# Kernel optimization log

Hardware: AMD Instinct MI355X
Metric: run time of the kernel (lower is better)

## Reference

```python
import jax, jax.numpy as jnp
import numpy as np

DIM = 7
HID = 128
BATCH = 131072
CHOL = DIM * (DIM + 1) // 2  # 28
_TRIL_R, _TRIL_C = np.tril_indices(DIM)
_DIAG = np.arange(DIM)


def _mlp(x, W1, b1, W2, b2, W3, b3):
    h = jnp.tanh(x @ W1 + b1)
    h = jnp.tanh(h @ W2 + b2)
    return h @ W3 + b3


def _build_cholesky(raw):
    # raw: [..., CHOL] -> lower-triangular L [..., DIM, DIM], softplus diagonal for positivity
    L = jnp.zeros(raw.shape[:-1] + (DIM, DIM), raw.dtype)
    L = L.at[..., _TRIL_R, _TRIL_C].set(raw)
    L = L.at[..., _DIAG, _DIAG].set(jax.nn.softplus(L[..., _DIAG, _DIAG]))
    return L


def _spd(raw):
    L = _build_cholesky(raw)
    return L @ jnp.swapaxes(L, -1, -2)  # L L^T, SPD


def setup_inputs() -> dict:
    key = jax.random.key(0)
    ks = jax.random.split(key, 20)
    s = 0.1
    f = jnp.float32
    return {
        "q": jax.random.normal(ks[0], (BATCH, DIM), f),
        "dq": jax.random.normal(ks[1], (BATCH, DIM), f),
        "ddq": jax.random.normal(ks[2], (BATCH, DIM), f),
        "mW1": jax.random.normal(ks[3], (DIM, HID), f) * s,
        "mb1": jax.random.normal(ks[4], (HID,), f) * s,
        "mW2": jax.random.normal(ks[5], (HID, HID), f) * s,
        "mb2": jax.random.normal(ks[6], (HID,), f) * s,
        "mW3": jax.random.normal(ks[7], (HID, CHOL), f) * s,
        "mb3": jax.random.normal(ks[8], (CHOL,), f) * s,
        "dW1": jax.random.normal(ks[9], (2 * DIM, HID), f) * s,
        "db1": jax.random.normal(ks[10], (HID,), f) * s,
        "dW2": jax.random.normal(ks[11], (HID, HID), f) * s,
        "db2": jax.random.normal(ks[12], (HID,), f) * s,
        "dW3": jax.random.normal(ks[13], (HID, CHOL), f) * s,
        "db3": jax.random.normal(ks[14], (CHOL,), f) * s,
        "pW1": jax.random.normal(ks[15], (DIM, HID), f) * s,
        "pb1": jax.random.normal(ks[16], (HID,), f) * s,
        "pw2": jax.random.normal(ks[17], (HID,), f) * s,
    }


def reference(q, dq, ddq, mW1, mb1, mW2, mb2, mW3, mb3,
              dW1, db1, dW2, db2, dW3, db3, pW1, pb1, pw2):
    def M_single(qi):  # qi: [DIM] -> [DIM, DIM]
        return _spd(_mlp(qi, mW1, mb1, mW2, mb2, mW3, mb3))

    # Mass matrix M(q): [B, DIM, DIM]
    Mb = _spd(_mlp(q, mW1, mb1, mW2, mb2, mW3, mb3))

    # Full batched Jacobian dM[i,k]/dq[j] -> J[b,i,k,j], replaces DIM^3 autograd.grad loop
    J = jax.vmap(jax.jacfwd(M_single))(q)  # [B, DIM, DIM, DIM]

    # Coriolis: C[b,i,j] = 0.5 * sum_k (dM_ik/dq_j + dM_ij/dq_k - dM_jk/dq_i) * dq_k
    C = 0.5 * (jnp.einsum('bikj,bk->bij', J, dq)
               + jnp.einsum('bijk,bk->bij', J, dq)
               - jnp.einsum('bjki,bk->bij', J, dq))

    # Damping D(q, dq): [B, DIM, DIM]
    Db = _spd(_mlp(jnp.concatenate([q, dq], axis=1), dW1, db1, dW2, db2, dW3, db3))

    # Convex potential (1-hidden-layer ICNN) and its gradient
    def V_single(qi):
        h = jax.nn.softplus(qi @ pW1 + pb1)
        return h @ jax.nn.softplus(pw2)

    gradV = jax.vmap(jax.grad(V_single))(q)  # [B, DIM]

    tau = (jnp.einsum('bij,bj->bi', Mb, ddq)
           + jnp.einsum('bij,bj->bi', C + Db, dq)
           + gradV)
    return tau
```

## Files before the change

### kernel.cpp

```cpp
#include <hip/hip_runtime.h>

#define DIM 7
#define HID 128
#define CHOL 28

#define GRID_A 256
#define ITER_A 16
#define GRID_B 256
#define ITER_B 4

#define PHASE_FENCE() __builtin_amdgcn_sched_barrier(0x7F)

typedef float    f32x4  __attribute__((ext_vector_type(4)));
typedef short    bf16x8 __attribute__((ext_vector_type(8)));
typedef unsigned uint4v __attribute__((ext_vector_type(4)));
typedef unsigned uint2v __attribute__((ext_vector_type(2)));

__device__ __forceinline__ float tanh_f(float x){ float e=__expf(2.f*x); return 1.f - 2.f/(e+1.f); }
__device__ __forceinline__ float sig_f(float x){ return 1.f/(1.f+__expf(-x)); }
__device__ __forceinline__ float sp_f(float x){ return fmaxf(x,0.f) + __logf(1.f+__expf(-fabsf(x))); }

__device__ __forceinline__ unsigned short f2b(float v){
  unsigned u = __float_as_uint(v);
  u += 0x7FFFu + ((u>>16)&1u);
  return (unsigned short)(u>>16);
}
__device__ __forceinline__ unsigned pk2(float a, float b){
  unsigned ua = __float_as_uint(a), ub = __float_as_uint(b);
  ua += 0x7FFFu + ((ua>>16)&1u);
  ub += 0x7FFFu + ((ub>>16)&1u);
  return (ua>>16) | (ub & 0xFFFF0000u);
}
__device__ __forceinline__ float b2f(unsigned short v){
  return __uint_as_float(((unsigned)v)<<16);
}
__device__ __forceinline__ bf16x8 as_bf(uint4v u){ union { uint4v a; bf16x8 f; } x; x.a=u; return x.f; }

__global__ void setup_frags(const float* __restrict__ mW2, const float* __restrict__ mW3,
                            const float* __restrict__ dW2, const float* __restrict__ dW3,
                            unsigned* __restrict__ ws){
  int idx = blockIdx.x*256 + threadIdx.x;
  if (idx < 8192) {
    int i2 = idx&3, f = idx>>2, l = f&63, st = f>>6;
    int s = st>>3, t = st&7;
    int k = 32*s + 8*(l>>4) + 2*i2, col = 16*t + (l&15);
    ws[idx] = pk2(mW2[k*HID+col], mW2[(k+1)*HID+col]);
  } else if (idx < 10240) {
    int j = idx-8192; int i2=j&3, f=j>>2, l=f&63, st=f>>6;
    int s = st>>1, t = st&1;
    int k = 32*s + 8*(l>>4) + 2*i2, col = 16*t + (l&15);
    float v0 = (col<CHOL) ? mW3[k*CHOL+col] : 0.f;
    float v1 = (col<CHOL) ? mW3[(k+1)*CHOL+col] : 0.f;
    ws[idx] = pk2(v0,v1);
  } else if (idx < 18432) {
    int j = idx-10240; int i2=j&3, f=j>>2, l=f&63, st=f>>6;
    int s = st>>3, t = st&7;
    int k = 32*s + 8*(l>>4) + 2*i2, col = 16*t + (l&15);
    ws[idx] = pk2(dW2[k*HID+col], dW2[(k+1)*HID+col]);
  } else if (idx < 20480) {
    int j = idx-18432; int i2=j&3, f=j>>2, l=f&63, st=f>>6;
    int s = st>>1, t = st&1;
    int k = 32*s + 8*(l>>4) + 2*i2, col = 16*t + (l&15);
    float v0 = (col<CHOL) ? dW3[k*CHOL+col] : 0.f;
    float v1 = (col<CHOL) ? dW3[(k+1)*CHOL+col] : 0.f;
    ws[idx] = pk2(v0,v1);
  }
}

__global__ __launch_bounds__(512, 2) void kernA(
    const float* __restrict__ q, const float* __restrict__ dq, const float* __restrict__ ddq,
    const float* __restrict__ mW1, const float* __restrict__ mb1,
    const float* __restrict__ mb2, const float* __restrict__ mb3,
    const float* __restrict__ pW1, const float* __restrict__ pb1, const float* __restrict__ pw2,
    const unsigned* __restrict__ ws, float* __restrict__ out)
{
  __shared__ __align__(16) unsigned short Abuf[8][2][16][HID];
  __shared__ __align__(16) uint4v W2lds[2048];
  __shared__ __align__(16) uint4v W3lds[512];
  __shared__ __align__(4)  unsigned short sbf[8][4][HID];
  __shared__ __align__(16) unsigned short rawb[8][4][CHOL][8];
  __shared__ float pW1s[DIM][HID+8];
  __shared__ float b2s[HID];
  __shared__ float b3s[CHOL];
  __shared__ float Lbs[8][4][CHOL], dLss[8][4][CHOL], dfs[8][4][CHOL];
  __shared__ float gvp2[8][4][14];
  __shared__ float wbs[8][4][DIM], ubs[8][4][DIM], vss[8][4][DIM];

  const int tid  = threadIdx.x;
  const int wid  = tid>>6;
  const int lane = tid&63;
  const int g4 = lane>>4, c = lane&15;
  const int R = lane&15, r7 = lane&7;

  if (tid < HID) b2s[tid] = mb2[tid];
  if (tid >= HID && tid < HID+CHOL) b3s[tid-HID] = mb3[tid-HID];
  for (int idx = tid; idx < DIM*HID; idx += 512) pW1s[idx>>7][idx&127] = pW1[idx];
  for (int idx = tid; idx < 2048; idx += 512) W2lds[idx] = ((const uint4v*)ws)[idx];
  for (int idx = tid; idx < 512;  idx += 512) W3lds[idx] = ((const uint4v*)(ws + 8192))[idx];

  const int u0 = 2*lane, u1 = 2*lane+1;
  float w1a[DIM], w1b[DIM], pw1a[DIM], pw1b[DIM];
#pragma unroll
  for (int j=0;j<DIM;++j){
    w1a[j]=mW1[j*HID+u0];  w1b[j]=mW1[j*HID+u1];
    pw1a[j]=pW1[j*HID+u0]; pw1b[j]=pW1[j*HID+u1];
  }
  const float b1a=mb1[u0], b1b=mb1[u1];
  const float pba=pb1[u0], pbb=pb1[u1];
  const float spa=sp_f(pw2[u0]), spb=sp_f(pw2[u1]);

  __syncthreads();

  const int kb = lane>>2;
  const int ko2 = (2*lane)&7;

  for (int it=0; it<ITER_A; ++it){
    const int ebase = (it*GRID_A + (int)blockIdx.x)*32 + wid*4;

#pragma unroll
    for (int e=0;e<4;++e){
      const float* qp = q + (long)(ebase+e)*DIM;
      float qv[DIM];
#pragma unroll
      for (int j=0;j<DIM;++j) qv[j]=qp[j];
      const int mt = e>>1, R0 = 8*(e&1);
      float z1a=b1a, z1b=b1b, zpa=pba, zpb=pbb;
#pragma unroll
      for (int j=0;j<DIM;++j){
        z1a=fmaf(qv[j],w1a[j],z1a);  z1b=fmaf(qv[j],w1b[j],z1b);
        zpa=fmaf(qv[j],pw1a[j],zpa); zpb=fmaf(qv[j],pw1b[j],zpb);
      }
      const float h1a=tanh_f(z1a), g1a=1.f-h1a*h1a;
      const float h1b=tanh_f(z1b), g1b=1.f-h1b*h1b;
      *(unsigned*)&Abuf[wid][mt][R0][8*kb + ko2] = pk2(h1a, h1b);
#pragma unroll
      for (int j=0;j<DIM;++j)
        *(unsigned*)&Abuf[wid][mt][R0+1+j][8*(kb^(1+j)) + ko2] = pk2(g1a*w1a[j], g1b*w1b[j]);
      *(unsigned*)&sbf[wid][e][u0] = pk2(sig_f(zpa)*spa, sig_f(zpb)*spb);
    }
    PHASE_FENCE();

    bf16x8 Af0[4], Af1[4];
#pragma unroll
    for (int s=0;s<4;++s){
      const int blk = 8*((4*s+g4)^r7);
      Af0[s] = *(const bf16x8*)&Abuf[wid][0][R][blk];
      Af1[s] = *(const bf16x8*)&Abuf[wid][1][R][blk];
    }
    PHASE_FENCE();

#pragma unroll
    for (int t=0;t<8;++t){
      f32x4 a0 = f32x4{0.f,0.f,0.f,0.f};
      f32x4 a1 = f32x4{0.f,0.f,0.f,0.f};
#pragma unroll
      for (int s=0;s<4;++s){
        bf16x8 B = as_bf(W2lds[(s*8+t)*64 + lane]);
        a0 = __builtin_amdgcn_mfma_f32_16x16x32_bf16(Af0[s],B,a0,0,0,0);
        a1 = __builtin_amdgcn_mfma_f32_16x16x32_bf16(Af1[s],B,a1,0,0,0);
      }
      const int col = 16*t+c;
      const int cb = col>>3, co = col&7;
      {
        const float z2  = a0[0] + b2s[col];
        const float h2o = tanh_f(z2);
        const float h2x = __shfl_xor(h2o, 16);
        const float h2  = (g4&1) ? h2x : h2o;
        const float g2  = 1.f - h2*h2;
#pragma unroll
        for (int reg=0;reg<4;++reg){
          const int Rr = 4*g4+reg;
          const int key = Rr&7;
          float v = g2*a0[reg];
          if (key==0) v = h2;
          Abuf[wid][0][Rr][8*(cb^key) + co] = f2b(v);
        }
      }
      {
        const float z2  = a1[0] + b2s[col];
        const float h2o = tanh_f(z2);
        const float h2x = __shfl_xor(h2o, 16);
        const float h2  = (g4&1) ? h2x : h2o;
        const float g2  = 1.f - h2*h2;
#pragma unroll
        for (int reg=0;reg<4;++reg){
          const int Rr = 4*g4+reg;
          const int key = Rr&7;
          float v = g2*a1[reg];
          if (key==0) v = h2;
          Abuf[wid][1][Rr][8*(cb^key) + co] = f2b(v);
        }
      }
    }
    PHASE_FENCE();

    f32x4 acc3[2][2];
#pragma unroll
    for (int a=0;a<2;++a){ acc3[a][0]=f32x4{0.f,0.f,0.f,0.f}; acc3[a][1]=f32x4{0.f,0.f,0.f,0.f}; }
#pragma unroll
    for (int s=0;s<4;++s){
      const int blk = 8*((4*s+g4)^r7);
      bf16x8 A0 = *(const bf16x8*)&Abuf[wid][0][R][blk];
      bf16x8 A1 = *(const bf16x8*)&Abuf[wid][1][R][blk];
#pragma unroll
      for (int nt=0;nt<2;++nt){
        bf16x8 B = as_bf(W3lds[(s*2+nt)*64 + lane]);
        acc3[0][nt] = __builtin_amdgcn_mfma_f32_16x16x32_bf16(A0,B,acc3[0][nt],0,0,0);
        acc3[1][nt] = __builtin_amdgcn_mfma_f32_16x16x32_bf16(A1,B,acc3[1][nt],0,0,0);
      }
    }

    if (c < 14){
      const int iv = (c<7)? c : c-7;
      const int nb = (c<7)? 0 : 64;
      float gp = 0.f;
#pragma unroll 8
      for (int nn=0; nn<32; ++nn){
        const unsigned sp2 = *(const unsigned*)&sbf[wid][g4][nb+2*nn];
        const float2 pw = *(const float2*)&pW1s[iv][nb+2*nn];
        gp = fmaf(pw.x, __uint_as_float(sp2<<16), gp);
        gp = fmaf(pw.y, __uint_as_float(sp2 & 0xFFFF0000u), gp);
      }
      gvp2[wid][g4][c] = gp;
    }

#pragma unroll
    for (int mt=0;mt<2;++mt){
      const int em = 2*mt + (g4>>1);
      const int rb = (g4&1)*4;
#pragma unroll
      for (int nt=0;nt<2;++nt){
        const int t = 16*nt+c;
        if (t < CHOL){
          uint2v p;
          p[0] = pk2(acc3[mt][nt][0], acc3[mt][nt][1]);
          p[1] = pk2(acc3[mt][nt][2], acc3[mt][nt][3]);
          *(uint2v*)&rawb[wid][em][t][rb] = p;
        }
      }
    }
    PHASE_FENCE();

    float dqv[DIM];
    {
      const float* dqp = dq + (long)(ebase+g4)*DIM;
#pragma unroll
      for (int j=0;j<DIM;++j) dqv[j]=dqp[j];
    }
#pragma unroll
    for (int h=0;h<2;++h){
      const int t = c + 16*h;
      if (t < CHOL){
        const uint4v r8 = *(const uint4v*)&rawb[wid][g4][t][0];
        const float rw0 = __uint_as_float(r8[0]<<16);
        const float rw1 = __uint_as_float(r8[0]&0xFFFF0000u);
        const float rw2 = __uint_as_float(r8[1]<<16);
        const float rw3 = __uint_as_float(r8[1]&0xFFFF0000u);
        const float rw4 = __uint_as_float(r8[2]<<16);
        const float rw5 = __uint_as_float(r8[2]&0xFFFF0000u);
        const float rw6 = __uint_as_float(r8[3]<<16);
        const float rw7 = __uint_as_float(r8[3]&0xFFFF0000u);
        const float e0 = rw0 + b3s[t];
        const bool dg = (t==0)|(t==2)|(t==5)|(t==9)|(t==14)|(t==20)|(t==27);
        const float Lv = dg ? sp_f(e0) : e0;
        const float df = dg ? sig_f(e0) : 1.f;
        float s_ = dqv[0]*rw1;
        s_ = fmaf(dqv[1], rw2, s_); s_ = fmaf(dqv[2], rw3, s_);
        s_ = fmaf(dqv[3], rw4, s_); s_ = fmaf(dqv[4], rw5, s_);
        s_ = fmaf(dqv[5], rw6, s_); s_ = fmaf(dqv[6], rw7, s_);
        Lbs[wid][g4][t]=Lv; dfs[wid][g4][t]=df; dLss[wid][g4][t]=df*s_;
      }
    }
    PHASE_FENCE();
    if (c < DIM){
      const float* ddqp = ddq + (long)(ebase+g4)*DIM;
      float wv=0.f, uv=0.f, vv=0.f;
#pragma unroll
      for (int r=0;r<DIM;++r){
        if (r>=c){
          const int id=r*(r+1)/2+c;
          const float Lrc = Lbs[wid][g4][id];
          wv=fmaf(Lrc,dqv[r],wv);
          uv=fmaf(Lrc,ddqp[r],uv);
          vv=fmaf(dLss[wid][g4][id],dqv[r],vv);
        }
      }
      wbs[wid][g4][c]=wv; ubs[wid][g4][c]=uv; vss[wid][g4][c]=vv;
    }
    PHASE_FENCE();
    if (c < DIM){
      const int i=c;
      float t12=0.f;
#pragma unroll
      for (int c2=0;c2<DIM;++c2){
        if (c2<=i){
          const int id=i*(i+1)/2+c2;
          t12=fmaf(Lbs[wid][g4][id], ubs[wid][g4][c2]+vss[wid][g4][c2], t12);
          t12=fmaf(dLss[wid][g4][id], wbs[wid][g4][c2], t12);
        }
      }
      const int TRt[CHOL]={0,1,1,2,2,2,3,3,3,3,4,4,4,4,4,5,5,5,5,5,5,6,6,6,6,6,6,6};
      const int TCt[CHOL]={0,0,1,0,1,2,0,1,2,3,0,1,2,3,4,0,1,2,3,4,5,0,1,2,3,4,5,6};
      float t3=0.f;
#pragma unroll
      for (int t=0;t<CHOL;++t)
        t3=fmaf(b2f(rawb[wid][g4][t][1+i])*dfs[wid][g4][t], dqv[TRt[t]]*wbs[wid][g4][TCt[t]], t3);
      out[(long)(ebase+g4)*DIM + i] = t12 - t3 + gvp2[wid][g4][i] + gvp2[wid][g4][7+i];
    }
    PHASE_FENCE();
  }
}

__global__ __launch_bounds__(512, 2) void kernB(
    const float* __restrict__ q, const float* __restrict__ dq,
    const float* __restrict__ dW1, const float* __restrict__ db1,
    const float* __restrict__ db2, const float* __restrict__ db3,
    const unsigned* __restrict__ ws, float* __restrict__ out)
{
  __shared__ __align__(16) unsigned short AbufD[8][16][HID];
  __shared__ __align__(16) uint4v dW2lds[2048];
  __shared__ __align__(16) uint4v dW3lds[512];
  __shared__ float dW1s[2*DIM][HID];
  __shared__ float xsf[8][112+8], dsf[8][112+8];
  __shared__ float rawD[8][16][CHOL];
  __shared__ float LbD[8][16][CHOL];
  __shared__ float wdb[8][16][8];
  __shared__ float b2sD[HID];
  __shared__ float b3sD[CHOL];

  const int tid  = threadIdx.x;
  const int wid  = tid>>6;
  const int lane = tid&63;
  const int g4 = lane>>4, c = lane&15;
  const int R = lane&15, rkey = lane&7;
  const int eL = lane>>2, sub = lane&3;

  if (tid < HID) b2sD[tid] = db2[tid];
  if (tid >= HID && tid < HID+CHOL) b3sD[tid-HID] = db3[tid-HID];
  for (int idx = tid; idx < 2*DIM*HID; idx += 512) dW1s[idx>>7][idx&127] = dW1[idx];
  for (int idx = tid; idx < 2048; idx += 512) dW2lds[idx] = ((const uint4v*)(ws + 10240))[idx];
  for (int idx = tid; idx < 512;  idx += 512) dW3lds[idx] = ((const uint4v*)(ws + 18432))[idx];
  const float b1v0 = db1[lane], b1v1 = db1[lane+64];

  __syncthreads();

  for (int it=0; it<ITER_B; ++it){
    const int ebase = (it*GRID_B + (int)blockIdx.x)*128 + wid*16;

    for (int idx=lane; idx<112; idx+=64){
      xsf[wid][idx] = q[(long)ebase*DIM + idx];
      dsf[wid][idx] = dq[(long)ebase*DIM + idx];
    }
    PHASE_FENCE();

#pragma unroll
    for (int h=0; h<2; ++h){
      const int k = lane + 64*h;
      float z[16];
#pragma unroll
      for (int e=0;e<16;++e) z[e] = h ? b1v1 : b1v0;
#pragma unroll
      for (int j=0;j<DIM;++j){
        const float dj = dW1s[j][k & 127];
#pragma unroll
        for (int e=0;e<16;++e) z[e] = fmaf(xsf[wid][7*e+j], dj, z[e]);
      }
#pragma unroll
      for (int j=0;j<DIM;++j){
        const float dj = dW1s[DIM+j][k & 127];
#pragma unroll
        for (int e=0;e<16;++e) z[e] = fmaf(dsf[wid][7*e+j], dj, z[e]);
      }
      const int kb2 = k>>3, ko = k&7;
#pragma unroll
      for (int e=0;e<16;++e){
        AbufD[wid][e][8*(kb2^(e&7)) + ko] = f2b(tanh_f(z[e]));
      }
    }
    PHASE_FENCE();

    f32x4 acc[8];
#pragma unroll
    for (int b=0;b<8;++b) acc[b] = f32x4{0.f,0.f,0.f,0.f};
#pragma unroll
    for (int s=0;s<4;++s){
      const int blk = 8*((4*s+g4)^rkey);
      bf16x8 A0 = *(const bf16x8*)&AbufD[wid][R][blk];
#pragma unroll
      for (int t=0;t<8;++t)
        acc[t] = __builtin_amdgcn_mfma_f32_16x16x32_bf16(A0, as_bf(dW2lds[(s*8+t)*64+lane]), acc[t], 0,0,0);
    }
    PHASE_FENCE();

#pragma unroll
    for (int t=0;t<8;++t){
      const int col = 16*t+c;
      const int cb = col>>3, co = col&7;
#pragma unroll
      for (int reg=0;reg<4;++reg){
        const int e = 4*g4+reg;
        const float h2 = tanh_f(acc[t][reg] + b2sD[col]);
        AbufD[wid][e][8*(cb^(e&7)) + co] = f2b(h2);
      }
    }
    PHASE_FENCE();

    f32x4 acc3[2];
    acc3[0]=f32x4{0.f,0.f,0.f,0.f}; acc3[1]=f32x4{0.f,0.f,0.f,0.f};
#pragma unroll
    for (int s=0;s<4;++s){
      const int blk = 8*((4*s+g4)^rkey);
      bf16x8 A0 = *(const bf16x8*)&AbufD[wid][R][blk];
#pragma unroll
      for (int nt=0;nt<2;++nt)
        acc3[nt] = __builtin_amdgcn_mfma_f32_16x16x32_bf16(A0, as_bf(dW3lds[(s*2+nt)*64+lane]), acc3[nt], 0,0,0);
    }

#pragma unroll
    for (int nt=0;nt<2;++nt){
      const int t = 16*nt+c;
      if (t < CHOL){
#pragma unroll
        for (int reg=0;reg<4;++reg) rawD[wid][4*g4+reg][t] = acc3[nt][reg];
      }
    }
    PHASE_FENCE();

#pragma unroll
    for (int m=0;m<7;++m){
      const int t = 7*sub + m;
      const float e0 = rawD[wid][eL][t] + b3sD[t];
      const bool dg = (t==0)|(t==2)|(t==5)|(t==9)|(t==14)|(t==20)|(t==27);
      LbD[wid][eL][t] = dg ? sp_f(e0) : e0;
    }
    PHASE_FENCE();

    for (int cc = sub; cc < DIM; cc += 4){
      float wv = 0.f;
      for (int r = cc; r < DIM; ++r)
        wv = fmaf(LbD[wid][eL][r*(r+1)/2 + cc], dsf[wid][7*eL + r], wv);
      wdb[wid][eL][cc] = wv;
    }
    PHASE_FENCE();

    for (int i0 = sub; i0 < DIM; i0 += 4){
      float td = 0.f;
      for (int cc = 0; cc <= i0; ++cc)
        td = fmaf(LbD[wid][eL][i0*(i0+1)/2 + cc], wdb[wid][eL][cc], td);
      out[(long)(ebase+eL)*DIM + i0] += td;
    }
    PHASE_FENCE();
  }
}

extern "C" void kernel_launch(void* const* d_in, const int* in_sizes, int n_in,
                              void* d_out, int out_size, void* d_ws, size_t ws_size,
                              hipStream_t stream) {
  const float* q   = (const float*)d_in[0];
  const float* dq  = (const float*)d_in[1];
  const float* ddq = (const float*)d_in[2];
  const float* mW1 = (const float*)d_in[3];
  const float* mb1 = (const float*)d_in[4];
  const float* mW2 = (const float*)d_in[5];
  const float* mb2 = (const float*)d_in[6];
  const float* mW3 = (const float*)d_in[7];
  const float* mb3 = (const float*)d_in[8];
  const float* dW1 = (const float*)d_in[9];
  const float* db1 = (const float*)d_in[10];
  const float* dW2 = (const float*)d_in[11];
  const float* db2 = (const float*)d_in[12];
  const float* dW3 = (const float*)d_in[13];
  const float* db3 = (const float*)d_in[14];
  const float* pW1 = (const float*)d_in[15];
  const float* pb1 = (const float*)d_in[16];
  const float* pw2 = (const float*)d_in[17];
  float* out = (float*)d_out;
  unsigned* wsu = (unsigned*)d_ws;

  hipLaunchKernelGGL(setup_frags, dim3(80), dim3(256), 0, stream, mW2, mW3, dW2, dW3, wsu);
  hipLaunchKernelGGL(kernA, dim3(GRID_A), dim3(512), 0, stream,
                     q, dq, ddq, mW1, mb1, mb2, mb3, pW1, pb1, pw2, (const unsigned*)wsu, out);
  hipLaunchKernelGGL(kernB, dim3(GRID_B), dim3(512), 0, stream,
                     q, dq, dW1, db1, db2, db3, (const unsigned*)wsu, out);
}
```

Before: 239.1 us.

## Hold W2 fragments in registers, halve per-wave elements, double kernA grid

kernA now keeps the full W2 B-operand fragments (32 uint4 per lane) in registers instead of LDS. Each wave processes 2 elements per iteration instead of 4, with one MFMA M-tile, and the grid doubles to keep total coverage. Shrinking LDS usage is meant to allow 4 blocks per CU and more latency hiding. The cost is heavy VGPR pressure from the 128-register W2 cache at the higher launch bound, which may cause spills, plus half the MFMA work per B load.

```diff
diff --git a/kernel.cpp b/kernel.cpp
--- a/kernel.cpp
+++ b/kernel.cpp
@@ -4,7 +4,7 @@
 #define HID 128
 #define CHOL 28
 
-#define GRID_A 256
+#define GRID_A 512
 #define ITER_A 16
 #define GRID_B 256
 #define ITER_B 4
@@ -67,35 +67,34 @@
   }
 }
 
-__global__ __launch_bounds__(512, 2) void kernA(
+__global__ __launch_bounds__(512, 4) void kernA(
     const float* __restrict__ q, const float* __restrict__ dq, const float* __restrict__ ddq,
     const float* __restrict__ mW1, const float* __restrict__ mb1,
     const float* __restrict__ mb2, const float* __restrict__ mb3,
     const float* __restrict__ pW1, const float* __restrict__ pb1, const float* __restrict__ pw2,
     const unsigned* __restrict__ ws, float* __restrict__ out)
 {
-  __shared__ __align__(16) unsigned short Abuf[8][2][16][HID];
-  __shared__ __align__(16) uint4v W2lds[2048];
+  __shared__ __align__(16) unsigned short Abuf[8][16][HID];
   __shared__ __align__(16) uint4v W3lds[512];
-  __shared__ __align__(4)  unsigned short sbf[8][4][HID];
-  __shared__ __align__(16) unsigned short rawb[8][4][CHOL][8];
+  __shared__ __align__(4)  unsigned short sbf[8][2][HID];
+  __shared__ __align__(16) unsigned short rawb[8][2][CHOL][8];
   __shared__ float pW1s[DIM][HID+8];
   __shared__ float b2s[HID];
   __shared__ float b3s[CHOL];
-  __shared__ float Lbs[8][4][CHOL], dLss[8][4][CHOL], dfs[8][4][CHOL];
-  __shared__ float gvp2[8][4][14];
-  __shared__ float wbs[8][4][DIM], ubs[8][4][DIM], vss[8][4][DIM];
+  __shared__ float Lbs[8][2][CHOL], dLss[8][2][CHOL], dfs[8][2][CHOL];
+  __shared__ float gvp2[8][2][14];
+  __shared__ float wbs[8][2][DIM], ubs[8][2][DIM], vss[8][2][DIM];
 
   const int tid  = threadIdx.x;
   const int wid  = tid>>6;
   const int lane = tid&63;
   const int g4 = lane>>4, c = lane&15;
   const int R = lane&15, r7 = lane&7;
+  const int emt = lane>>5, s5 = lane&31;
 
   if (tid < HID) b2s[tid] = mb2[tid];
   if (tid >= HID && tid < HID+CHOL) b3s[tid-HID] = mb3[tid-HID];
   for (int idx = tid; idx < DIM*HID; idx += 512) pW1s[idx>>7][idx&127] = pW1[idx];
-  for (int idx = tid; idx < 2048; idx += 512) W2lds[idx] = ((const uint4v*)ws)[idx];
   for (int idx = tid; idx < 512;  idx += 512) W3lds[idx] = ((const uint4v*)(ws + 8192))[idx];
 
   const int u0 = 2*lane, u1 = 2*lane+1;
@@ -109,21 +108,26 @@
   const float pba=pb1[u0], pbb=pb1[u1];
   const float spa=sp_f(pw2[u0]), spb=sp_f(pw2[u1]);
 
+  const uint4v* __restrict__ W2f = (const uint4v*)ws;
+  uint4v W2r[32];
+#pragma unroll
+  for (int i=0;i<32;++i) W2r[i] = W2f[i*64 + lane];
+
   __syncthreads();
 
   const int kb = lane>>2;
   const int ko2 = (2*lane)&7;
 
   for (int it=0; it<ITER_A; ++it){
-    const int ebase = (it*GRID_A + (int)blockIdx.x)*32 + wid*4;
-
-#pragma unroll
-    for (int e=0;e<4;++e){
+    const int ebase = (it*GRID_A + (int)blockIdx.x)*16 + wid*2;
+
+#pragma unroll
+    for (int e=0;e<2;++e){
       const float* qp = q + (long)(ebase+e)*DIM;
       float qv[DIM];
 #pragma unroll
       for (int j=0;j<DIM;++j) qv[j]=qp[j];
-      const int mt = e>>1, R0 = 8*(e&1);
+      const int R0 = 8*e;
       float z1a=b1a, z1b=b1b, zpa=pba, zpb=pbb;
 #pragma unroll
       for (int j=0;j<DIM;++j){
@@ -132,109 +136,80 @@
       }
       const float h1a=tanh_f(z1a), g1a=1.f-h1a*h1a;
       const float h1b=tanh_f(z1b), g1b=1.f-h1b*h1b;
-      *(unsigned*)&Abuf[wid][mt][R0][8*kb + ko2] = pk2(h1a, h1b);
+      *(unsigned*)&Abuf[wid][R0][8*kb + ko2] = pk2(h1a, h1b);
 #pragma unroll
       for (int j=0;j<DIM;++j)
-        *(unsigned*)&Abuf[wid][mt][R0+1+j][8*(kb^(1+j)) + ko2] = pk2(g1a*w1a[j], g1b*w1b[j]);
+        *(unsigned*)&Abuf[wid][R0+1+j][8*(kb^(1+j)) + ko2] = pk2(g1a*w1a[j], g1b*w1b[j]);
       *(unsigned*)&sbf[wid][e][u0] = pk2(sig_f(zpa)*spa, sig_f(zpb)*spb);
     }
     PHASE_FENCE();
 
-    bf16x8 Af0[4], Af1[4];
+    bf16x8 Af[4];
 #pragma unroll
     for (int s=0;s<4;++s){
       const int blk = 8*((4*s+g4)^r7);
-      Af0[s] = *(const bf16x8*)&Abuf[wid][0][R][blk];
-      Af1[s] = *(const bf16x8*)&Abuf[wid][1][R][blk];
+      Af[s] = *(const bf16x8*)&Abuf[wid][R][blk];
     }
     PHASE_FENCE();
 
 #pragma unroll
     for (int t=0;t<8;++t){
       f32x4 a0 = f32x4{0.f,0.f,0.f,0.f};
-      f32x4 a1 = f32x4{0.f,0.f,0.f,0.f};
-#pragma unroll
-      for (int s=0;s<4;++s){
-        bf16x8 B = as_bf(W2lds[(s*8+t)*64 + lane]);
-        a0 = __builtin_amdgcn_mfma_f32_16x16x32_bf16(Af0[s],B,a0,0,0,0);
-        a1 = __builtin_amdgcn_mfma_f32_16x16x32_bf16(Af1[s],B,a1,0,0,0);
-      }
+#pragma unroll
+      for (int s=0;s<4;++s)
+        a0 = __builtin_amdgcn_mfma_f32_16x16x32_bf16(Af[s], as_bf(W2r[s*8+t]), a0, 0,0,0);
       const int col = 16*t+c;
       const int cb = col>>3, co = col&7;
-      {
-        const float z2  = a0[0] + b2s[col];
-        const float h2o = tanh_f(z2);
-        const float h2x = __shfl_xor(h2o, 16);
-        const float h2  = (g4&1) ? h2x : h2o;
-        const float g2  = 1.f - h2*h2;
-#pragma unroll
-        for (int reg=0;reg<4;++reg){
-          const int Rr = 4*g4+reg;
-          const int key = Rr&7;
-          float v = g2*a0[reg];
-          if (key==0) v = h2;
-          Abuf[wid][0][Rr][8*(cb^key) + co] = f2b(v);
-        }
-      }
-      {
-        const float z2  = a1[0] + b2s[col];
-        const float h2o = tanh_f(z2);
-        const float h2x = __shfl_xor(h2o, 16);
-        const float h2  = (g4&1) ? h2x : h2o;
-        const float g2  = 1.f - h2*h2;
-#pragma unroll
-        for (int reg=0;reg<4;++reg){
-          const int Rr = 4*g4+reg;
-          const int key = Rr&7;
-          float v = g2*a1[reg];
-          if (key==0) v = h2;
-          Abuf[wid][1][Rr][8*(cb^key) + co] = f2b(v);
-        }
-      }
-    }
-    PHASE_FENCE();
-
-    f32x4 acc3[2][2];
-#pragma unroll
-    for (int a=0;a<2;++a){ acc3[a][0]=f32x4{0.f,0.f,0.f,0.f}; acc3[a][1]=f32x4{0.f,0.f,0.f,0.f}; }
+      const float z2  = a0[0] + b2s[col];
+      const float h2o = tanh_f(z2);
+      const float h2x = __shfl_xor(h2o, 16);
+      const float h2  = (g4&1) ? h2x : h2o;
+      const float g2  = 1.f - h2*h2;
+#pragma unroll
+      for (int reg=0;reg<4;++reg){
+        const int Rr = 4*g4+reg;
+        const int key = Rr&7;
+        float v = g2*a0[reg];
+        if (key==0) v = h2;
+        Abuf[wid][Rr][8*(cb^key) + co] = f2b(v);
+      }
+    }
+    PHASE_FENCE();
+
+    f32x4 acc3[2];
+    acc3[0]=f32x4{0.f,0.f,0.f,0.f}; acc3[1]=f32x4{0.f,0.f,0.f,0.f};
 #pragma unroll
     for (int s=0;s<4;++s){
       const int blk = 8*((4*s+g4)^r7);
-      bf16x8 A0 = *(const bf16x8*)&Abuf[wid][0][R][blk];
-      bf16x8 A1 = *(const bf16x8*)&Abuf[wid][1][R][blk];
-#pragma unroll
-      for (int nt=0;nt<2;++nt){
-        bf16x8 B = as_bf(W3lds[(s*2+nt)*64 + lane]);
-        acc3[0][nt] = __builtin_amdgcn_mfma_f32_16x16x32_bf16(A0,B,acc3[0][nt],0,0,0);
-        acc3[1][nt] = __builtin_amdgcn_mfma_f32_16x16x32_bf16(A1,B,acc3[1][nt],0,0,0);
-      }
-    }
-
-    if (c < 14){
-      const int iv = (c<7)? c : c-7;
-      const int nb = (c<7)? 0 : 64;
+      bf16x8 A0 = *(const bf16x8*)&Abuf[wid][R][blk];
+#pragma unroll
+      for (int nt=0;nt<2;++nt)
+        acc3[nt] = __builtin_amdgcn_mfma_f32_16x16x32_bf16(A0, as_bf(W3lds[(s*2+nt)*64+lane]), acc3[nt], 0,0,0);
+    }
+
+    if (s5 < 14){
+      const int iv = (s5<7)? s5 : s5-7;
+      const int nb = (s5<7)? 0 : 64;
       float gp = 0.f;
 #pragma unroll 8
       for (int nn=0; nn<32; ++nn){
-        const unsigned sp2 = *(const unsigned*)&sbf[wid][g4][nb+2*nn];
+        const unsigned sp2 = *(const unsigned*)&sbf[wid][emt][nb+2*nn];
         const float2 pw = *(const float2*)&pW1s[iv][nb+2*nn];
         gp = fmaf(pw.x, __uint_as_float(sp2<<16), gp);
         gp = fmaf(pw.y, __uint_as_float(sp2 & 0xFFFF0000u), gp);
       }
-      gvp2[wid][g4][c] = gp;
-    }
-
-#pragma unroll
-    for (int mt=0;mt<2;++mt){
-      const int em = 2*mt + (g4>>1);
-      const int rb = (g4&1)*4;
+      gvp2[wid][emt][s5] = gp;
+    }
+
+    {
+      const int em = g4>>1, rb = 4*(g4&1);
 #pragma unroll
       for (int nt=0;nt<2;++nt){
         const int t = 16*nt+c;
         if (t < CHOL){
           uint2v p;
-          p[0] = pk2(acc3[mt][nt][0], acc3[mt][nt][1]);
-          p[1] = pk2(acc3[mt][nt][2], acc3[mt][nt][3]);
+          p[0] = pk2(acc3[nt][0], acc3[nt][1]);
+          p[1] = pk2(acc3[nt][2], acc3[nt][3]);
           *(uint2v*)&rawb[wid][em][t][rb] = p;
         }
       }
@@ -243,60 +218,58 @@
 
     float dqv[DIM];
     {
-      const float* dqp = dq + (long)(ebase+g4)*DIM;
+      const float* dqp = dq + (long)(ebase+emt)*DIM;
 #pragma unroll
       for (int j=0;j<DIM;++j) dqv[j]=dqp[j];
     }
-#pragma unroll
-    for (int h=0;h<2;++h){
-      const int t = c + 16*h;
-      if (t < CHOL){
-        const uint4v r8 = *(const uint4v*)&rawb[wid][g4][t][0];
-        const float rw0 = __uint_as_float(r8[0]<<16);
-        const float rw1 = __uint_as_float(r8[0]&0xFFFF0000u);
-        const float rw2 = __uint_as_float(r8[1]<<16);
-        const float rw3 = __uint_as_float(r8[1]&0xFFFF0000u);
-        const float rw4 = __uint_as_float(r8[2]<<16);
-        const float rw5 = __uint_as_float(r8[2]&0xFFFF0000u);
-        const float rw6 = __uint_as_float(r8[3]<<16);
-        const float rw7 = __uint_as_float(r8[3]&0xFFFF0000u);
-        const float e0 = rw0 + b3s[t];
-        const bool dg = (t==0)|(t==2)|(t==5)|(t==9)|(t==14)|(t==20)|(t==27);
-        const float Lv = dg ? sp_f(e0) : e0;
-        const float df = dg ? sig_f(e0) : 1.f;
-        float s_ = dqv[0]*rw1;
-        s_ = fmaf(dqv[1], rw2, s_); s_ = fmaf(dqv[2], rw3, s_);
-        s_ = fmaf(dqv[3], rw4, s_); s_ = fmaf(dqv[4], rw5, s_);
-        s_ = fmaf(dqv[5], rw6, s_); s_ = fmaf(dqv[6], rw7, s_);
-        Lbs[wid][g4][t]=Lv; dfs[wid][g4][t]=df; dLss[wid][g4][t]=df*s_;
-      }
-    }
-    PHASE_FENCE();
-    if (c < DIM){
-      const float* ddqp = ddq + (long)(ebase+g4)*DIM;
+    if (s5 < CHOL){
+      const int t = s5;
+      const uint4v r8 = *(const uint4v*)&rawb[wid][emt][t][0];
+      const float rw0 = __uint_as_float(r8[0]<<16);
+      const float rw1 = __uint_as_float(r8[0]&0xFFFF0000u);
+      const float rw2 = __uint_as_float(r8[1]<<16);
+      const float rw3 = __uint_as_float(r8[1]&0xFFFF0000u);
+      const float rw4 = __uint_as_float(r8[2]<<16);
+      const float rw5 = __uint_as_float(r8[2]&0xFFFF0000u);
+      const float rw6 = __uint_as_float(r8[3]<<16);
+      const float rw7 = __uint_as_float(r8[3]&0xFFFF0000u);
+      const float e0 = rw0 + b3s[t];
+      const bool dg = (t==0)|(t==2)|(t==5)|(t==9)|(t==14)|(t==20)|(t==27);
+      const float Lv = dg ? sp_f(e0) : e0;
+      const float df = dg ? sig_f(e0) : 1.f;
+      float s_ = dqv[0]*rw1;
+      s_ = fmaf(dqv[1], rw2, s_); s_ = fmaf(dqv[2], rw3, s_);
+      s_ = fmaf(dqv[3], rw4, s_); s_ = fmaf(dqv[4], rw5, s_);
+      s_ = fmaf(dqv[5], rw6, s_); s_ = fmaf(dqv[6], rw7, s_);
+      Lbs[wid][emt][t]=Lv; dfs[wid][emt][t]=df; dLss[wid][emt][t]=df*s_;
+    }
+    PHASE_FENCE();
+    if (s5 < DIM){
+      const int cc = s5;
+      const float* ddqp = ddq + (long)(ebase+emt)*DIM;
       float wv=0.f, uv=0.f, vv=0.f;
 #pragma unroll
       for (int r=0;r<DIM;++r){
-        if (r>=c){
-          const int id=r*(r+1)/2+c;
-          const float Lrc = Lbs[wid][g4][id];
+        if (r>=cc){
+          const int id=r*(r+1)/2+cc;
+          const float Lrc = Lbs[wid][emt][id];
           wv=fmaf(Lrc,dqv[r],wv);
           uv=fmaf(Lrc,ddqp[r],uv);
-          vv=fmaf(dLss[wid][g4][id],dqv[r],vv);
+          vv=fmaf(dLss[wid][emt][id],dqv[r],vv);
         }
       }
-      wbs[wid][g4][c]=wv; ubs[wid][g4][c]=uv; vss[wid][g4][c]=vv;
-    }
-    PHASE_FENCE();
-    if (c < DIM){
-      const int i=c;
+      wbs[wid][emt][cc]=wv; ubs[wid][emt][cc]=uv; vss[wid][emt][cc]=vv;
+    }
+    PHASE_FENCE();
+    if (s5 < DIM){
+      const int i=s5;
       float t12=0.f;
 #pragma unroll
       for (int c2=0;c2<DIM;++c2){
         if (c2<=i){
           const int id=i*(i+1)/2+c2;
-          t12=fmaf(Lbs[wid][g4][id], ubs[wid][g4][c2]+vss[wid][g4][c2], t12);
-          t12=fmaf(dLss[wid][g4][id], wbs[wid][g4][c2], t12);
+          t12=fmaf(Lbs[wid][emt][id], ubs[wid][emt][c2]+vss[wid][emt][c2], t12);
+          t12=fmaf(dLss[wid][emt][id], wbs[wid][emt][c2], t12);
         }
       }
       const int TRt[CHOL]={0,1,1,2,2,2,3,3,3,3,4,4,4,4,4,5,5,5,5,5,5,6,6,6,6,6,6,6};
@@ -304,8 +277,8 @@
       float t3=0.f;
 #pragma unroll
       for (int t=0;t<CHOL;++t)
-        t3=fmaf(b2f(rawb[wid][g4][t][1+i])*dfs[wid][g4][t], dqv[TRt[t]]*wbs[wid][g4][TCt[t]], t3);
-      out[(long)(ebase+g4)*DIM + i] = t12 - t3 + gvp2[wid][g4][i] + gvp2[wid][g4][7+i];
+        t3=fmaf(b2f(rawb[wid][emt][t][1+i])*dfs[wid][emt][t], dqv[TRt[t]]*wbs[wid][emt][TCt[t]], t3);
+      out[(long)(ebase+emt)*DIM + i] = t12 - t3 + gvp2[wid][emt][i] + gvp2[wid][emt][7+i];
     }
     PHASE_FENCE();
   }
```

Measured after the change: 545.1 us. 128% more time.
